# Optimization experiments

Hardware: AMD Instinct MI355X
Metric: run time of the kernel (lower is better)

Reference implementation:

```python
import jax, jax.numpy as jnp
import numpy as np

EPS = 1e-12  # matches F.normalize default eps


def _l2_normalize(x):
    n = jnp.linalg.norm(x, axis=-1, keepdims=True)
    return x / jnp.maximum(n, EPS)


def setup_inputs() -> dict:
    key = jax.random.key(0)
    k1, k2, k3 = jax.random.split(key, 3)
    B, N, DK, DV = 1024, 131072, 256, 256
    return {
        "query": jax.random.normal(k1, (B, DK), dtype=jnp.float32),
        "keys": jax.random.normal(k2, (N, DK), dtype=jnp.float32),
        "values": jax.random.normal(k3, (N, DV), dtype=jnp.float32),
        "valid": jnp.ones((N,), dtype=bool),
        "top_k": 8,
    }


def reference(query, keys, values, valid, top_k):
    # Cosine-similarity top-k retrieval (LongMemKVCache.retrieve with a full buffer).
    q_norm = _l2_normalize(query)            # [B, dk]
    k_norm = _l2_normalize(keys)             # [N, dk]
    sim = q_norm @ k_norm.T                  # [B, N]
    # Invalid slots can never be selected (fancy-index filter in the original).
    sim = jnp.where(valid[None, :], sim, -jnp.inf)
    _, idx = jax.lax.top_k(sim, top_k)       # [B, K]
    gathered_keys = keys[idx]                # [B, K, dk]
    gathered_vals = values[idx]              # [B, K, dv]
    return gathered_keys, gathered_vals
```

## Files before the change

### kernel.cpp

```cpp
#include <hip/hip_runtime.h>
#include <math.h>


#define B_Q 1024
#define N_K 131072
#define DIM 256
#define TOPK 8
#define G_KEYS 1024
#define N_GROUPS (N_K / G_KEYS)
#define CAND 16
#define P_PER_G 16
#define P_PER_Q (N_GROUPS * P_PER_G)

typedef short bf16x8 __attribute__((ext_vector_type(8)));
typedef float floatx4 __attribute__((ext_vector_type(4)));
typedef const __attribute__((address_space(1))) unsigned int* gas_u32;
typedef __attribute__((address_space(3))) unsigned int* las_u32;

#define PL64 8192
#define SMEM_SHORTS 16896
#define DUMP_PITCH 132

#define FB_PITCH 40
#define FB_AH 0
#define FB_AL 5120
#define FB_BH 10240
#define FB_BL 15360
#define FB_SMEM 20480
#define FB_DUMP_PITCH 132

__device__ __forceinline__ unsigned short bf16_hi(float x) {
    return (unsigned short)(__float_as_uint(x) >> 16);
}
__device__ __forceinline__ float hi_part(float x) {
    return __uint_as_float(__float_as_uint(x) & 0xffff0000u);
}
__device__ __forceinline__ unsigned int umin_(unsigned int a, unsigned int b) {
    return a < b ? a : b;
}
__device__ __forceinline__ unsigned int umax_(unsigned int a, unsigned int b) {
    return a > b ? a : b;
}
__device__ __forceinline__ unsigned int mono(float v) {
    unsigned int u = __float_as_uint(v);
    return u ^ ((unsigned int)((int)u >> 31) | 0x80000000u);
}
__device__ __forceinline__ void ins_packed(unsigned int* t, float v, unsigned int idx) {
    unsigned int k = (mono(v) & 0xFFFFFC00u) | idx;
    #pragma unroll
    for (int j = 7; j > 0; --j) t[j] = umax_(t[j], umin_(t[j - 1], k));
    t[0] = umax_(t[0], k);
}

__global__ __launch_bounds__(256)
void norms_kernel(const float* __restrict__ keys, float* __restrict__ invk) {
    const int row  = blockIdx.x * 4 + (threadIdx.x >> 6);
    const int lane = threadIdx.x & 63;
    const float4* k4 = (const float4*)keys;
    const float4 v = k4[row * 64 + lane];
    float s = v.x * v.x + v.y * v.y + v.z * v.z + v.w * v.w;
    #pragma unroll
    for (int off = 32; off; off >>= 1) s += __shfl_down(s, off);
    if (lane == 0) invk[row] = 1.0f / fmaxf(sqrtf(s), 1e-12f);
}

__global__ __launch_bounds__(256)
void prep_kernel(const float* __restrict__ qry, const float* __restrict__ keys,
                 unsigned short* __restrict__ KH, unsigned short* __restrict__ QH) {
    __shared__ float linv[128];
    const int bx = blockIdx.x;
    const int tid = threadIdx.x;
    const bool is_q = bx >= 1024;
    const int t0 = is_q ? (bx - 1024) : bx;
    const float4* src4 = (const float4*)(is_q ? qry : keys);
    unsigned short* H = is_q ? QH : KH;

    if (!is_q) {
        const int r  = tid >> 1;
        const int hf = tid & 1;
        const float4* row4 = &src4[(t0 * 128 + r) * 64 + hf * 32];
        float s = 0.0f;
        #pragma unroll
        for (int i = 0; i < 32; ++i) {
            const float4 v = row4[i];
            s += v.x * v.x + v.y * v.y + v.z * v.z + v.w * v.w;
        }
        s += __shfl_xor(s, 1);
        if (hf == 0) linv[r] = 1.0f / fmaxf(sqrtf(s), 1e-12f);
        __syncthreads();
    }

    #pragma unroll
    for (int i = 0; i < 32; ++i) {
        const int f = i * 256 + tid;
        const int dc = f >> 10;
        const int r  = (f & 1023) >> 3;
        const int db = f & 7;
        float4 v = src4[(t0 * 128 + r) * 64 + dc * 8 + db];
        if (!is_q) {
            const float iv = linv[r];
            v.x *= iv; v.y *= iv; v.z *= iv; v.w *= iv;
        }
        const size_t o = (size_t)(t0 * 8 + dc) * 4096 + r * 32 + db * 4;
        *(ushort4*)&H[o] = make_ushort4(bf16_hi(v.x), bf16_hi(v.y),
                                        bf16_hi(v.z), bf16_hi(v.w));
    }
}

__global__ __launch_bounds__(256, 4)
void sim_topk_kernel(const unsigned short* __restrict__ QH,
                     const unsigned short* __restrict__ KH,
                     unsigned int* __restrict__ part) {
    __shared__ __align__(16) unsigned short smem[SMEM_SHORTS];
    float* smemf = (float*)smem;

    const int tid  = threadIdx.x;
    const int w    = tid >> 6;
    const int lane = tid & 63;
    const int quad = lane >> 4;
    const int m16  = tid & 15;
    const int bxg  = blockIdx.x;
    const int by   = blockIdx.y;
    const int qb   = (w >> 1) * 64;
    const int kb   = (w & 1) * 64;

    const int qq = tid & 127;
    const int sg = tid >> 7;
    const int qhalf = qq >> 6;

    unsigned int t8[8];
    #pragma unroll
    for (int i = 0; i < 8; ++i) t8[i] = 0u;

    unsigned short* ldst = &smem[w * 4096];

    for (int tile = 0; tile < 8; ++tile) {
        floatx4 acc[4][4];
        #pragma unroll
        for (int i = 0; i < 4; ++i)
            #pragma unroll
            for (int j = 0; j < 4; ++j) acc[i][j] = (floatx4)0.0f;

        for (int dc2 = 0; dc2 < 4; ++dc2) {
            const unsigned short* gsrc =
                (w < 2) ? &QH[(size_t)(by * 8 + dc2 * 2 + w) * 4096]
                        : &KH[(size_t)((bxg * 8 + tile) * 8 + dc2 * 2 + (w - 2)) * 4096];
            #pragma unroll
            for (int s = 0; s < 8; ++s) {
                __builtin_amdgcn_global_load_lds(
                    (gas_u32)(gsrc + s * 512 + lane * 8),
                    (las_u32)(ldst + s * 512), 16, 0, 0);
            }
            __syncthreads();

            #pragma unroll
            for (int c = 0; c < 2; ++c) {
                bf16x8 ah[4];
                #pragma unroll
                for (int i = 0; i < 4; ++i)
                    ah[i] = *(const bf16x8*)&smem[c * 4096 + (qb + 16 * i + m16) * 32 + 8 * quad];
                #pragma unroll
                for (int j = 0; j < 4; ++j) {
                    const bf16x8 bh = *(const bf16x8*)&smem[PL64 + c * 4096 +
                                                            (kb + 16 * j + m16) * 32 + 8 * quad];
                    #pragma unroll
                    for (int i = 0; i < 4; ++i)
                        acc[i][j] = __builtin_amdgcn_mfma_f32_16x16x32_bf16(ah[i], bh, acc[i][j], 0, 0, 0);
                }
            }
            __syncthreads();
        }

        for (int h = 0; h < 2; ++h) {
            if ((w >> 1) == h) {
                #pragma unroll
                for (int i = 0; i < 4; ++i)
                    #pragma unroll
                    for (int j = 0; j < 4; ++j)
                        #pragma unroll
                        for (int r = 0; r < 4; ++r)
                            smemf[(16 * i + 4 * quad + r) * DUMP_PITCH +
                                  kb + 16 * j + m16] = acc[i][j][r];
            }
            __syncthreads();
            if (qhalf == h) {
                const int row = qq & 63;
                const unsigned int ibase = (unsigned int)(tile * 128 + sg * 64);
                const float4* src = (const float4*)&smemf[row * DUMP_PITCH + sg * 64];
                #pragma unroll
                for (int s = 0; s < 16; ++s) {
                    const float4 sv = src[s];
                    ins_packed(t8, sv.x, ibase + s * 4 + 0);
                    ins_packed(t8, sv.y, ibase + s * 4 + 1);
                    ins_packed(t8, sv.z, ibase + s * 4 + 2);
                    ins_packed(t8, sv.w, ibase + s * 4 + 3);
                }
            }
            __syncthreads();
        }
    }

    unsigned int* dst = &part[((size_t)(by * 128 + qq) * N_GROUPS + bxg) * P_PER_G + sg * 8];
    *(uint4*)dst       = make_uint4(t8[0], t8[1], t8[2], t8[3]);
    *((uint4*)dst + 1) = make_uint4(t8[4], t8[5], t8[6], t8[7]);
}

__global__ __launch_bounds__(256, 3)
void sim_topk_fb(const float* __restrict__ qry, const float* __restrict__ keys,
                 const float* __restrict__ invk,
                 unsigned int* __restrict__ part) {
    __shared__ __align__(16) unsigned short smem[FB_SMEM];
    float* smemf = (float*)smem;

    const int tid  = threadIdx.x;
    const int w    = tid >> 6;
    const int quad = (tid & 63) >> 4;
    const int m16  = tid & 15;
    const int bxg  = blockIdx.x;
    const int q0   = blockIdx.y * 128;
    const int qb   = (w >> 1) * 64;
    const int kb   = (w & 1) * 64;
    const int qq   = tid & 127;
    const int sg   = tid >> 7;
    const int qhalf = qq >> 6;

    unsigned int t8[8];
    #pragma unroll
    for (int i = 0; i < 8; ++i) t8[i] = 0u;

    const float4* q4 = (const float4*)qry;
    const float4* k4 = (const float4*)keys;

    for (int tile = 0; tile < 8; ++tile) {
        const int k0 = bxg * G_KEYS + tile * 128;
        floatx4 acc[4][4];
        #pragma unroll
        for (int i = 0; i < 4; ++i)
            #pragma unroll
            for (int j = 0; j < 4; ++j) acc[i][j] = (floatx4)0.0f;

        for (int dc = 0; dc < 8; ++dc) {
            #pragma unroll
            for (int i = 0; i < 4; ++i) {
                const int f  = tid + 256 * i;
                const int r  = f >> 3;
                const int db = f & 7;
                const int lo = r * FB_PITCH + db * 4;
                const float4 av = q4[(q0 + r) * 64 + dc * 8 + db];
                {
                    float4 h = make_float4(hi_part(av.x), hi_part(av.y),
                                           hi_part(av.z), hi_part(av.w));
                    *(ushort4*)&smem[FB_AH + lo] = make_ushort4(bf16_hi(av.x), bf16_hi(av.y),
                                                                bf16_hi(av.z), bf16_hi(av.w));
                    *(ushort4*)&smem[FB_AL + lo] = make_ushort4(bf16_hi(av.x - h.x), bf16_hi(av.y - h.y),
                                                                bf16_hi(av.z - h.z), bf16_hi(av.w - h.w));
                }
                const float iv = invk[k0 + r];
                const float4 kv = k4[(k0 + r) * 64 + dc * 8 + db];
                {
                    const float bx = kv.x * iv, by2 = kv.y * iv,
                                bz = kv.z * iv, bw = kv.w * iv;
                    float4 h = make_float4(hi_part(bx), hi_part(by2),
                                           hi_part(bz), hi_part(bw));
                    *(ushort4*)&smem[FB_BH + lo] = make_ushort4(bf16_hi(bx), bf16_hi(by2),
                                                                bf16_hi(bz), bf16_hi(bw));
                    *(ushort4*)&smem[FB_BL + lo] = make_ushort4(bf16_hi(bx - h.x), bf16_hi(by2 - h.y),
                                                                bf16_hi(bz - h.z), bf16_hi(bw - h.w));
                }
            }
            __syncthreads();
            bf16x8 ah[4], al[4];
            #pragma unroll
            for (int i = 0; i < 4; ++i) {
                const int ro = (qb + 16 * i + m16) * FB_PITCH + 8 * quad;
                ah[i] = *(const bf16x8*)&smem[FB_AH + ro];
                al[i] = *(const bf16x8*)&smem[FB_AL + ro];
            }
            #pragma unroll
            for (int j = 0; j < 4; ++j) {
                const int ro = (kb + 16 * j + m16) * FB_PITCH + 8 * quad;
                const bf16x8 bh = *(const bf16x8*)&smem[FB_BH + ro];
                const bf16x8 bl = *(const bf16x8*)&smem[FB_BL + ro];
                #pragma unroll
                for (int i = 0; i < 4; ++i) {
                    acc[i][j] = __builtin_amdgcn_mfma_f32_16x16x32_bf16(ah[i], bh, acc[i][j], 0, 0, 0);
                    acc[i][j] = __builtin_amdgcn_mfma_f32_16x16x32_bf16(ah[i], bl, acc[i][j], 0, 0, 0);
                    acc[i][j] = __builtin_amdgcn_mfma_f32_16x16x32_bf16(al[i], bh, acc[i][j], 0, 0, 0);
                }
            }
            __syncthreads();
        }
        for (int h = 0; h < 2; ++h) {
            if ((w >> 1) == h) {
                #pragma unroll
                for (int i = 0; i < 4; ++i)
                    #pragma unroll
                    for (int j = 0; j < 4; ++j)
                        #pragma unroll
                        for (int r = 0; r < 4; ++r)
                            smemf[(16 * i + 4 * quad + r) * FB_DUMP_PITCH +
                                  kb + 16 * j + m16] = acc[i][j][r];
            }
            __syncthreads();
            if (qhalf == h) {
                const int row = qq & 63;
                const unsigned int ibase = (unsigned int)(tile * 128 + sg * 64);
                const float4* src = (const float4*)&smemf[row * FB_DUMP_PITCH + sg * 64];
                #pragma unroll
                for (int s = 0; s < 16; ++s) {
                    const float4 sv = src[s];
                    ins_packed(t8, sv.x, ibase + s * 4 + 0);
                    ins_packed(t8, sv.y, ibase + s * 4 + 1);
                    ins_packed(t8, sv.z, ibase + s * 4 + 2);
                    ins_packed(t8, sv.w, ibase + s * 4 + 3);
                }
            }
            __syncthreads();
        }
    }

    unsigned int* dst = &part[((size_t)(q0 + qq) * N_GROUPS + bxg) * P_PER_G + sg * 8];
    *(uint4*)dst       = make_uint4(t8[0], t8[1], t8[2], t8[3]);
    *((uint4*)dst + 1) = make_uint4(t8[4], t8[5], t8[6], t8[7]);
}

__global__ __launch_bounds__(256)
void select_kernel(const float* __restrict__ qry, const float* __restrict__ keys,
                   const float* __restrict__ vals,
                   const unsigned int* __restrict__ part,
                   float* __restrict__ out) {
    __shared__ unsigned int ck[P_PER_Q + 8];
    __shared__ unsigned int wrv[4];
    __shared__ int wrp[4];
    __shared__ unsigned int selk[CAND];
    __shared__ int selp[CAND];
    __shared__ double resv[CAND];
    __shared__ int    resi[CAND];
    __shared__ int    sel8[TOPK];

    const int tid = threadIdx.x;
    const int q = blockIdx.x;

    #pragma unroll
    for (int i = 0; i < 8; ++i)
        ck[tid * 8 + i] = part[(size_t)q * P_PER_Q + tid * 8 + i];
    if (tid < 8) ck[P_PER_Q + tid] = 0u;
    __syncthreads();

    int ptr = 0;
    for (int it = 0; it < CAND; ++it) {
        unsigned int bv = ck[tid * 8 + ptr];
        int bp = tid * 8 + ptr;
        #pragma unroll
        for (int off = 32; off; off >>= 1) {
            const unsigned int ov = __shfl_down(bv, off);
            const int          op = __shfl_down(bp, off);
            if (ov > bv) { bv = ov; bp = op; }
        }
        if ((tid & 63) == 0) { wrv[tid >> 6] = bv; wrp[tid >> 6] = bp; }
        __syncthreads();
        unsigned int mbv = wrv[0]; int mbp = wrp[0];
        #pragma unroll
        for (int ww = 1; ww < 4; ++ww)
            if (wrv[ww] > mbv) { mbv = wrv[ww]; mbp = wrp[ww]; }
        if (tid == 0) { selk[it] = mbv; selp[it] = mbp; }
        if ((mbp >> 3) == tid) ++ptr;
        __syncthreads();
    }

    const int wid = tid >> 6, lane = tid & 63;
    const float4 qv = ((const float4*)qry)[q * 64 + lane];
    for (int c = wid; c < CAND; c += 4) {
        const int kidx = (selp[c] >> 4) * G_KEYS + (int)(selk[c] & 1023u);
        const float4 kv = ((const float4*)keys)[kidx * 64 + lane];
        double dt = (double)qv.x * kv.x + (double)qv.y * kv.y +
                    (double)qv.z * kv.z + (double)qv.w * kv.w;
        double nm = (double)kv.x * kv.x + (double)kv.y * kv.y +
                    (double)kv.z * kv.z + (double)kv.w * kv.w;
        #pragma unroll
        for (int off = 32; off; off >>= 1) {
            dt += __shfl_down(dt, off);
            nm += __shfl_down(nm, off);
        }
        if (lane == 0) {
            resv[c] = dt / fmax(sqrt(nm), 1e-12);
            resi[c] = kidx;
        }
    }
    __syncthreads();

    if (tid == 0) {
        bool used[CAND];
        for (int c = 0; c < CAND; ++c) used[c] = false;
        for (int j = 0; j < TOPK; ++j) {
            int best = -1;
            for (int c = 0; c < CAND; ++c) {
                if (used[c]) continue;
                if (best < 0 || resv[c] > resv[best] ||
                    (resv[c] == resv[best] && resi[c] < resi[best]))
                    best = c;
            }
            used[best] = true;
            sel8[j] = resi[best];
        }
    }
    __syncthreads();

    const int kv_off = B_Q * TOPK * DIM;
    #pragma unroll
    for (int j = 0; j < TOPK; ++j) {
        const int id = sel8[j];
        const int o = (q * TOPK + j) * DIM + tid;
        out[o] = keys[id * DIM + tid];
        out[kv_off + o] = vals[id * DIM + tid];
    }
}

extern "C" void kernel_launch(void* const* d_in, const int* in_sizes, int n_in,
                              void* d_out, int out_size, void* d_ws, size_t ws_size,
                              hipStream_t stream) {
    const float* qry  = (const float*)d_in[0];
    const float* keys = (const float*)d_in[1];
    const float* vals = (const float*)d_in[2];
    float* out = (float*)d_out;

    unsigned int* part = (unsigned int*)d_ws;
    unsigned short* QH = (unsigned short*)(part + (size_t)B_Q * P_PER_Q);
    unsigned short* KH = QH + (size_t)B_Q * DIM;
    float* invk = (float*)(KH + (size_t)N_K * DIM);
    const size_t need = (size_t)((char*)(invk + N_K) - (char*)d_ws);

    if (ws_size >= need) {
        hipLaunchKernelGGL(prep_kernel, dim3(1032), dim3(256), 0, stream,
                           qry, keys, KH, QH);
        hipLaunchKernelGGL(sim_topk_kernel, dim3(N_GROUPS, B_Q / 128), dim3(256), 0, stream,
                           QH, KH, part);
    } else {
        hipLaunchKernelGGL(norms_kernel, dim3(N_K / 4), dim3(256), 0, stream,
                           keys, invk);
        hipLaunchKernelGGL(sim_topk_fb, dim3(N_GROUPS, B_Q / 128), dim3(256), 0, stream,
                           qry, keys, invk, part);
    }
    hipLaunchKernelGGL(select_kernel, dim3(B_Q), dim3(256), 0, stream,
                       qry, keys, vals, part, out);
}
```

Measured before the change: 459.6 us.

## Swizzle LDS layouts, split top-8 into two top-4 lists, cheaper keys

Adds an XOR swizzle to the bf16 operand planes written by the prep kernel and read from LDS by the MFMA loop. It replaces the padded dump buffer with an XOR-swizzled layout, aiming to cut LDS bank conflicts and LDS footprint. The per-thread top-8 insertion becomes two top-4 lists with a cheaper sort key (v+32 bit pattern). The merge kernel walks both sublists, and the prep norm loop is rewritten as per-wave row reductions. Keeping only four candidates per 32-key half could drop true top-k entries, which the candidate stage must tolerate.

After: 538.4 us. 1.17x slower.

```diff
diff --git a/kernel.cpp b/kernel.cpp
--- a/kernel.cpp
+++ b/kernel.cpp
@@ -18,8 +18,7 @@
 typedef __attribute__((address_space(3))) unsigned int* las_u32;
 
 #define PL64 8192
-#define SMEM_SHORTS 16896
-#define DUMP_PITCH 132
+#define SMEM_SHORTS 16384
 
 #define FB_PITCH 40
 #define FB_AH 0
@@ -50,6 +49,16 @@
     #pragma unroll
     for (int j = 7; j > 0; --j) t[j] = umax_(t[j], umin_(t[j - 1], k));
     t[0] = umax_(t[0], k);
+}
+__device__ __forceinline__ void ins4(unsigned int* t, float v, unsigned int idx) {
+    unsigned int k = (__float_as_uint(v + 32.0f) & 0xFFFFFC00u) | idx;
+    t[3] = umax_(t[3], umin_(t[2], k));
+    t[2] = umax_(t[2], umin_(t[1], k));
+    t[1] = umax_(t[1], umin_(t[0], k));
+    t[0] = umax_(t[0], k);
+}
+__device__ __forceinline__ int plane_swz(int row) {
+    return ((row ^ (row >> 2)) & 3);
 }
 
 __global__ __launch_bounds__(256)
@@ -76,17 +85,15 @@
     unsigned short* H = is_q ? QH : KH;
 
     if (!is_q) {
-        const int r  = tid >> 1;
-        const int hf = tid & 1;
-        const float4* row4 = &src4[(t0 * 128 + r) * 64 + hf * 32];
-        float s = 0.0f;
-        #pragma unroll
-        for (int i = 0; i < 32; ++i) {
-            const float4 v = row4[i];
-            s += v.x * v.x + v.y * v.y + v.z * v.z + v.w * v.w;
-        }
-        s += __shfl_xor(s, 1);
-        if (hf == 0) linv[r] = 1.0f / fmaxf(sqrtf(s), 1e-12f);
+        const int wv = tid >> 6, lane = tid & 63;
+        for (int k = 0; k < 32; ++k) {
+            const int r = k * 4 + wv;
+            const float4 v = src4[(size_t)(t0 * 128 + r) * 64 + lane];
+            float s = v.x * v.x + v.y * v.y + v.z * v.z + v.w * v.w;
+            #pragma unroll
+            for (int off = 32; off; off >>= 1) s += __shfl_down(s, off);
+            if (lane == 0) linv[r] = 1.0f / fmaxf(sqrtf(s), 1e-12f);
+        }
         __syncthreads();
     }
 
@@ -101,7 +108,8 @@
             const float iv = linv[r];
             v.x *= iv; v.y *= iv; v.z *= iv; v.w *= iv;
         }
-        const size_t o = (size_t)(t0 * 8 + dc) * 4096 + r * 32 + db * 4;
+        const int byte = (r * 64 + db * 8) ^ (plane_swz(r) << 4);
+        const size_t o = (size_t)(t0 * 8 + dc) * 4096 + (byte >> 1);
         *(ushort4*)&H[o] = make_ushort4(bf16_hi(v.x), bf16_hi(v.y),
                                         bf16_hi(v.z), bf16_hi(v.w));
     }
@@ -128,9 +136,9 @@
     const int sg = tid >> 7;
     const int qhalf = qq >> 6;
 
-    unsigned int t8[8];
-    #pragma unroll
-    for (int i = 0; i < 8; ++i) t8[i] = 0u;
+    unsigned int ta[4], tb[4];
+    #pragma unroll
+    for (int i = 0; i < 4; ++i) { ta[i] = 0u; tb[i] = 0u; }
 
     unsigned short* ldst = &smem[w * 4096];
 
@@ -157,12 +165,16 @@
             for (int c = 0; c < 2; ++c) {
                 bf16x8 ah[4];
                 #pragma unroll
-                for (int i = 0; i < 4; ++i)
-                    ah[i] = *(const bf16x8*)&smem[c * 4096 + (qb + 16 * i + m16) * 32 + 8 * quad];
+                for (int i = 0; i < 4; ++i) {
+                    const int row = qb + 16 * i + m16;
+                    const int qs = quad ^ plane_swz(row);
+                    ah[i] = *(const bf16x8*)&smem[c * 4096 + row * 32 + 8 * qs];
+                }
                 #pragma unroll
                 for (int j = 0; j < 4; ++j) {
-                    const bf16x8 bh = *(const bf16x8*)&smem[PL64 + c * 4096 +
-                                                            (kb + 16 * j + m16) * 32 + 8 * quad];
+                    const int row = kb + 16 * j + m16;
+                    const int qs = quad ^ plane_swz(row);
+                    const bf16x8 bh = *(const bf16x8*)&smem[PL64 + c * 4096 + row * 32 + 8 * qs];
                     #pragma unroll
                     for (int i = 0; i < 4; ++i)
                         acc[i][j] = __builtin_amdgcn_mfma_f32_16x16x32_bf16(ah[i], bh, acc[i][j], 0, 0, 0);
@@ -176,24 +188,30 @@
                 #pragma unroll
                 for (int i = 0; i < 4; ++i)
                     #pragma unroll
-                    for (int j = 0; j < 4; ++j)
+                    for (int j = 0; j < 4; ++j) {
+                        const int colg = (kb >> 2) + 4 * j + (m16 >> 2);
+                        const int e = m16 & 3;
                         #pragma unroll
-                        for (int r = 0; r < 4; ++r)
-                            smemf[(16 * i + 4 * quad + r) * DUMP_PITCH +
-                                  kb + 16 * j + m16] = acc[i][j][r];
+                        for (int r = 0; r < 4; ++r) {
+                            const int row = 16 * i + 4 * quad + r;
+                            smemf[(row << 7) + ((colg ^ (row & 7)) << 2) + e] = acc[i][j][r];
+                        }
+                    }
             }
             __syncthreads();
             if (qhalf == h) {
                 const int row = qq & 63;
+                const int rx = row & 7;
                 const unsigned int ibase = (unsigned int)(tile * 128 + sg * 64);
-                const float4* src = (const float4*)&smemf[row * DUMP_PITCH + sg * 64];
                 #pragma unroll
                 for (int s = 0; s < 16; ++s) {
-                    const float4 sv = src[s];
-                    ins_packed(t8, sv.x, ibase + s * 4 + 0);
-                    ins_packed(t8, sv.y, ibase + s * 4 + 1);
-                    ins_packed(t8, sv.z, ibase + s * 4 + 2);
-                    ins_packed(t8, sv.w, ibase + s * 4 + 3);
+                    const float4 sv = *(const float4*)
+                        &smemf[(row << 7) + ((((sg << 4) + s) ^ rx) << 2)];
+                    unsigned int* t = (s < 8) ? ta : tb;
+                    ins4(t, sv.x, ibase + s * 4 + 0);
+                    ins4(t, sv.y, ibase + s * 4 + 1);
+                    ins4(t, sv.z, ibase + s * 4 + 2);
+                    ins4(t, sv.w, ibase + s * 4 + 3);
                 }
             }
             __syncthreads();
@@ -201,8 +219,8 @@
     }
 
     unsigned int* dst = &part[((size_t)(by * 128 + qq) * N_GROUPS + bxg) * P_PER_G + sg * 8];
-    *(uint4*)dst       = make_uint4(t8[0], t8[1], t8[2], t8[3]);
-    *((uint4*)dst + 1) = make_uint4(t8[4], t8[5], t8[6], t8[7]);
+    *(uint4*)dst       = make_uint4(ta[0], ta[1], ta[2], ta[3]);
+    *((uint4*)dst + 1) = make_uint4(tb[0], tb[1], tb[2], tb[3]);
 }
 
 __global__ __launch_bounds__(256, 3)
@@ -347,10 +365,12 @@
     if (tid < 8) ck[P_PER_Q + tid] = 0u;
     __syncthreads();
 
-    int ptr = 0;
+    int p0 = 0, p1 = 0;
     for (int it = 0; it < CAND; ++it) {
-        unsigned int bv = ck[tid * 8 + ptr];
-        int bp = tid * 8 + ptr;
+        const unsigned int h0 = (p0 < 4) ? ck[tid * 8 + p0] : 0u;
+        const unsigned int h1 = (p1 < 4) ? ck[tid * 8 + 4 + p1] : 0u;
+        unsigned int bv = umax_(h0, h1);
+        int bp = tid * 8 + (h0 >= h1 ? p0 : 4 + p1);
         #pragma unroll
         for (int off = 32; off; off >>= 1) {
             const unsigned int ov = __shfl_down(bv, off);
@@ -364,7 +384,9 @@
         for (int ww = 1; ww < 4; ++ww)
             if (wrv[ww] > mbv) { mbv = wrv[ww]; mbp = wrp[ww]; }
         if (tid == 0) { selk[it] = mbv; selp[it] = mbp; }
-        if ((mbp >> 3) == tid) ++ptr;
+        if ((mbp >> 3) == tid) {
+            if ((mbp & 7) < 4) ++p0; else ++p1;
+        }
         __syncthreads();
     }
 
```
